# Kernel optimization log

Hardware: AMD Instinct MI355X
Metric: run time of the kernel (lower is better)

Reference implementation:

```python
import jax, jax.numpy as jnp
import numpy as np

D = 1024        # hidden_dim
E = 8           # num_experts
K = 2           # activated_experts
H = 4 * D       # ffn hidden


def setup_inputs() -> dict:
    key = jax.random.key(0)
    ks = jax.random.split(key, 12)
    s = 1.0 / np.sqrt(D)
    sh = 1.0 / np.sqrt(H)
    return {
        "x": jax.random.normal(ks[0], (2, 2048, D), dtype=jnp.float32),
        "gate_w": jax.random.uniform(ks[1], (D, E), minval=-s, maxval=s, dtype=jnp.float32),
        "gate_b": jax.random.uniform(ks[2], (E,), minval=-s, maxval=s, dtype=jnp.float32),
        "route_bias": jnp.zeros((E,), dtype=jnp.float32),
        "shared_w1": jax.random.uniform(ks[3], (D, H), minval=-s, maxval=s, dtype=jnp.float32),
        "shared_b1": jax.random.uniform(ks[4], (H,), minval=-s, maxval=s, dtype=jnp.float32),
        "shared_w2": jax.random.uniform(ks[5], (H, D), minval=-sh, maxval=sh, dtype=jnp.float32),
        "shared_b2": jax.random.uniform(ks[6], (D,), minval=-sh, maxval=sh, dtype=jnp.float32),
        "exp_w1": jax.random.uniform(ks[7], (E, D, H), minval=-s, maxval=s, dtype=jnp.float32),
        "exp_b1": jax.random.uniform(ks[8], (E, H), minval=-s, maxval=s, dtype=jnp.float32),
        "exp_w2": jax.random.uniform(ks[9], (E, H, D), minval=-sh, maxval=sh, dtype=jnp.float32),
        "exp_b2": jax.random.uniform(ks[10], (E, D), minval=-sh, maxval=sh, dtype=jnp.float32),
    }


def reference(x, gate_w, gate_b, route_bias, shared_w1, shared_b1, shared_w2,
              shared_b2, exp_w1, exp_b1, exp_w2, exp_b2):
    B, S, _ = x.shape
    xf = x.reshape(-1, D)                                  # [T, D]
    T = xf.shape[0]

    # Routing: gate logits + learned load-balancing bias -> softmax -> top-k
    gate_logits = xf @ gate_w + gate_b + route_bias        # [T, E]
    gate_probs = jax.nn.softmax(gate_logits, axis=-1)
    topk_p, topk_i = jax.lax.top_k(gate_probs, K)          # [T, K]
    topk_p = topk_p / jnp.sum(topk_p, axis=-1, keepdims=True)

    # Per-token combine weights over experts (zero for unselected experts)
    w = jnp.zeros((T, E), dtype=xf.dtype)
    w = w.at[jnp.arange(T)[:, None], topk_i].add(topk_p)   # [T, E]

    # Dense per-expert FFN (grouped GEMM form), weighted combine
    h = jax.nn.gelu(jnp.einsum('td,edh->eth', xf, exp_w1) + exp_b1[:, None, :],
                    approximate=False)                     # [E, T, H]
    y = jnp.einsum('eth,ehd->etd', h, exp_w2) + exp_b2[:, None, :]  # [E, T, D]
    combined = jnp.einsum('etd,te->td', y, w)              # [T, D]

    # Shared expert
    sh = jax.nn.gelu(xf @ shared_w1 + shared_b1, approximate=False)
    shared_out = sh @ shared_w2 + shared_b2                # [T, D]

    return (shared_out + combined).reshape(B, S, D)
```

## Files before the change

kernel.cpp:

```cpp
#include <hip/hip_runtime.h>
#include <math.h>

#define TT 4096
#define DD 1024
#define EE 8
#define HH 4096
#define NEXP 9

typedef __bf16 bf16;
typedef __bf16 bf16x4 __attribute__((ext_vector_type(4)));
typedef __bf16 bf16x8 __attribute__((ext_vector_type(8)));
typedef float  f32x4  __attribute__((ext_vector_type(4)));

#define GLOAD_LDS16(gptr, lptr)                                                   \
  __builtin_amdgcn_global_load_lds(                                               \
      (const __attribute__((address_space(1))) void*)(gptr),                      \
      (__attribute__((address_space(3))) void*)(lptr), 16, 0, 0)

__global__ void k_init(const float* __restrict__ x, bf16* __restrict__ xb,
                       float* __restrict__ out, int* __restrict__ counts,
                       int* __restrict__ cursors) {
  int i = blockIdx.x * blockDim.x + threadIdx.x;
  if (i < TT * DD) { xb[i] = (bf16)x[i]; out[i] = 0.0f; }
  if (i < EE) { counts[i] = 0; cursors[i] = 0; }
}

__global__ void k_route(const float* __restrict__ x, const float* __restrict__ gw,
                        const float* __restrict__ gb, const float* __restrict__ rb,
                        int* __restrict__ counts, int* __restrict__ tke,
                        float* __restrict__ tkp) {
  int gid = blockIdx.x * blockDim.x + threadIdx.x;
  int t = gid >> 6;
  int lane = gid & 63;
  if (t >= TT) return;
  const float* xt = x + (size_t)t * DD;
  float acc[EE];
#pragma unroll
  for (int e = 0; e < EE; e++) acc[e] = 0.f;
  for (int d = lane; d < DD; d += 64) {
    float xv = xt[d];
    const float* g = gw + (size_t)d * EE;
#pragma unroll
    for (int e = 0; e < EE; e++) acc[e] += xv * g[e];
  }
#pragma unroll
  for (int off = 32; off > 0; off >>= 1) {
#pragma unroll
    for (int e = 0; e < EE; e++) acc[e] += __shfl_down(acc[e], off);
  }
  if (lane == 0) {
    float l[EE];
#pragma unroll
    for (int e = 0; e < EE; e++) l[e] = acc[e] + gb[e] + rb[e];
    int i1 = 0;
#pragma unroll
    for (int e = 1; e < EE; e++) if (l[e] > l[i1]) i1 = e;
    int i2 = (i1 == 0) ? 1 : 0;
#pragma unroll
    for (int e = 0; e < EE; e++) if (e != i1 && l[e] > l[i2]) i2 = e;
    float e2 = expf(l[i2] - l[i1]);
    float s = 1.f + e2;
    tke[t * 2 + 0] = i1; tkp[t * 2 + 0] = 1.f / s;
    tke[t * 2 + 1] = i2; tkp[t * 2 + 1] = e2 / s;
    atomicAdd(&counts[i1], 1);
    atomicAdd(&counts[i2], 1);
  }
}

__global__ void k_prefix(const int* __restrict__ counts, int* __restrict__ expBase,
                         int* __restrict__ expCnt) {
  if (blockIdx.x == 0 && threadIdx.x == 0) {
    int off = TT;
    for (int e = 0; e < EE; e++) { expBase[e] = off; expCnt[e] = counts[e]; off += counts[e]; }
    expBase[8] = 0; expCnt[8] = TT;
  }
}

__global__ void k_scatter(const int* __restrict__ tke, const float* __restrict__ tkp,
                          const int* __restrict__ expBase, int* __restrict__ cursors,
                          int* __restrict__ rowTok, float* __restrict__ rowW) {
  int t = blockIdx.x * blockDim.x + threadIdx.x;
  if (t >= TT) return;
  rowTok[t] = t; rowW[t] = 1.f;
#pragma unroll
  for (int k = 0; k < 2; k++) {
    int e = tke[t * 2 + k];
    float p = tkp[t * 2 + k];
    int slot = atomicAdd(&cursors[e], 1);
    int r = expBase[e] + slot;
    rowTok[r] = t; rowW[r] = p;
  }
}

__global__ void k_wt(const float* __restrict__ expW, const float* __restrict__ shW,
                     bf16* __restrict__ outT, int K, int N) {
  __shared__ float t[64][65];
  int z = blockIdx.z;
  const float* W = (z == 8) ? shW : expW + (size_t)z * K * N;
  bf16* O = outT + (size_t)z * K * N;
  int n0 = blockIdx.x * 64, k0 = blockIdx.y * 64;
  int tid = threadIdx.x;
  int rr = tid >> 4;
  int cc = (tid & 15) * 4;
#pragma unroll
  for (int p = 0; p < 4; p++) {
    int k = p * 16 + rr;
    f32x4 v = *(const f32x4*)&W[(size_t)(k0 + k) * N + n0 + cc];
    t[k][cc + 0] = v[0]; t[k][cc + 1] = v[1]; t[k][cc + 2] = v[2]; t[k][cc + 3] = v[3];
  }
  __syncthreads();
#pragma unroll
  for (int p = 0; p < 4; p++) {
    int n = p * 16 + rr;
    bf16x4 o;
#pragma unroll
    for (int i = 0; i < 4; i++) o[i] = (bf16)t[cc + i][n];
    *(bf16x4*)&O[(size_t)(n0 + n) * K + k0 + cc] = o;
  }
}

__global__ __launch_bounds__(256, 2) void k_gemm1(
    const bf16* __restrict__ xb, const bf16* __restrict__ wt1,
    const float* __restrict__ sb1, const float* __restrict__ eb1,
    const int* __restrict__ rowTok, const int* __restrict__ expBase,
    const int* __restrict__ expCnt, bf16* __restrict__ hbuf) {
  int ex = blockIdx.z;
  int base = expBase[ex];
  int cnt  = expCnt[ex];
  int mt = blockIdx.y;
  if (mt * 128 >= cnt) return;
  int n0 = blockIdx.x * 128;
  const bf16* Bt = wt1 + (size_t)ex * HH * DD;
  const float* b1 = (ex == 8) ? sb1 : eb1 + (size_t)ex * HH;

  __shared__ bf16 As[128 * 32];
  __shared__ bf16 Bs[128 * 32];
  __shared__ int  toks[128];

  int tid = threadIdx.x;
  int lane = tid & 63;
  int wv = tid >> 6;
  int wm = (wv & 1) * 64;
  int wn = (wv >> 1) * 64;

  if (tid < 128) {
    int rr = min(mt * 128 + tid, cnt - 1);
    toks[tid] = rowTok[base + rr];
  }

  f32x4 acc[4][4];
#pragma unroll
  for (int a = 0; a < 4; a++)
#pragma unroll
    for (int b = 0; b < 4; b++) acc[a][b] = (f32x4){0.f, 0.f, 0.f, 0.f};

  __syncthreads();

  int r0 = wv * 32 + (lane >> 2);
  int c8 = (lane & 3) * 8;

  for (int k0 = 0; k0 < DD; k0 += 32) {
    GLOAD_LDS16(xb + (size_t)toks[r0] * DD + k0 + c8,      As + wv * 1024);
    GLOAD_LDS16(xb + (size_t)toks[r0 + 16] * DD + k0 + c8, As + wv * 1024 + 512);
    GLOAD_LDS16(Bt + (size_t)(n0 + r0) * DD + k0 + c8,      Bs + wv * 1024);
    GLOAD_LDS16(Bt + (size_t)(n0 + r0 + 16) * DD + k0 + c8, Bs + wv * 1024 + 512);
    __syncthreads();
    bf16x8 af[4], bfr[4];
#pragma unroll
    for (int mi = 0; mi < 4; mi++)
      af[mi] = *(const bf16x8*)&As[(wm + mi * 16 + (lane & 15)) * 32 + (lane >> 4) * 8];
#pragma unroll
    for (int ni = 0; ni < 4; ni++)
      bfr[ni] = *(const bf16x8*)&Bs[(wn + ni * 16 + (lane & 15)) * 32 + (lane >> 4) * 8];
#pragma unroll
    for (int mi = 0; mi < 4; mi++)
#pragma unroll
      for (int ni = 0; ni < 4; ni++)
        acc[mi][ni] = __builtin_amdgcn_mfma_f32_16x16x32_bf16(af[mi], bfr[ni], acc[mi][ni], 0, 0, 0);
    __syncthreads();
  }

  int rsub = (lane >> 4) * 4;
#pragma unroll
  for (int ni = 0; ni < 4; ni++) {
    int col = n0 + wn + ni * 16 + (lane & 15);
    float bias = b1[col];
#pragma unroll
    for (int mi = 0; mi < 4; mi++) {
#pragma unroll
      for (int r = 0; r < 4; r++) {
        int mrow = mt * 128 + wm + mi * 16 + rsub + r;
        if (mrow < cnt) {
          float v = acc[mi][ni][r] + bias;
          v = 0.5f * v * (1.f + erff(v * 0.70710678118654752f));
          hbuf[(size_t)(base + mrow) * HH + col] = (bf16)v;
        }
      }
    }
  }
}

__global__ __launch_bounds__(256, 2) void k_gemm2(
    const bf16* __restrict__ hbuf, const bf16* __restrict__ wt2,
    const float* __restrict__ sb2, const float* __restrict__ eb2,
    const int* __restrict__ rowTok, const float* __restrict__ rowW,
    const int* __restrict__ expBase, const int* __restrict__ expCnt,
    float* __restrict__ out) {
  int ex = blockIdx.z;
  int base = expBase[ex];
  int cnt  = expCnt[ex];
  int mt = blockIdx.y;
  if (mt * 128 >= cnt) return;
  int n0 = blockIdx.x * 128;
  const bf16* Bt = wt2 + (size_t)ex * DD * HH;
  const float* b2 = (ex == 8) ? sb2 : eb2 + (size_t)ex * DD;

  __shared__ bf16 As[128 * 32];
  __shared__ bf16 Bs[128 * 32];
  __shared__ int   toks[128];
  __shared__ float wrow[128];

  int tid = threadIdx.x;
  int lane = tid & 63;
  int wv = tid >> 6;
  int wm = (wv & 1) * 64;
  int wn = (wv >> 1) * 64;

  if (tid < 128) {
    int rr = min(mt * 128 + tid, cnt - 1);
    toks[tid] = rowTok[base + rr];
    wrow[tid] = rowW[base + rr];
  }

  f32x4 acc[4][4];
#pragma unroll
  for (int a = 0; a < 4; a++)
#pragma unroll
    for (int b = 0; b < 4; b++) acc[a][b] = (f32x4){0.f, 0.f, 0.f, 0.f};

  __syncthreads();

  int r0 = wv * 32 + (lane >> 2);
  int c8 = (lane & 3) * 8;
  int pr0 = base + min(mt * 128 + r0, cnt - 1);
  int pr1 = base + min(mt * 128 + r0 + 16, cnt - 1);
  const bf16* ga0 = hbuf + (size_t)pr0 * HH + c8;
  const bf16* ga1 = hbuf + (size_t)pr1 * HH + c8;

  for (int k0 = 0; k0 < HH; k0 += 32) {
    GLOAD_LDS16(ga0 + k0, As + wv * 1024);
    GLOAD_LDS16(ga1 + k0, As + wv * 1024 + 512);
    GLOAD_LDS16(Bt + (size_t)(n0 + r0) * HH + k0 + c8,      Bs + wv * 1024);
    GLOAD_LDS16(Bt + (size_t)(n0 + r0 + 16) * HH + k0 + c8, Bs + wv * 1024 + 512);
    __syncthreads();
    bf16x8 af[4], bfr[4];
#pragma unroll
    for (int mi = 0; mi < 4; mi++)
      af[mi] = *(const bf16x8*)&As[(wm + mi * 16 + (lane & 15)) * 32 + (lane >> 4) * 8];
#pragma unroll
    for (int ni = 0; ni < 4; ni++)
      bfr[ni] = *(const bf16x8*)&Bs[(wn + ni * 16 + (lane & 15)) * 32 + (lane >> 4) * 8];
#pragma unroll
    for (int mi = 0; mi < 4; mi++)
#pragma unroll
      for (int ni = 0; ni < 4; ni++)
        acc[mi][ni] = __builtin_amdgcn_mfma_f32_16x16x32_bf16(af[mi], bfr[ni], acc[mi][ni], 0, 0, 0);
    __syncthreads();
  }

  int rsub = (lane >> 4) * 4;
#pragma unroll
  for (int ni = 0; ni < 4; ni++) {
    int col = n0 + wn + ni * 16 + (lane & 15);
    float bias = b2[col];
#pragma unroll
    for (int mi = 0; mi < 4; mi++) {
#pragma unroll
      for (int r = 0; r < 4; r++) {
        int local = wm + mi * 16 + rsub + r;
        int mrow = mt * 128 + local;
        if (mrow < cnt) {
          float v = acc[mi][ni][r] + bias;
          atomicAdd(&out[(size_t)toks[local] * DD + col], wrow[local] * v);
        }
      }
    }
  }
}

extern "C" void kernel_launch(void* const* d_in, const int* in_sizes, int n_in,
                              void* d_out, int out_size, void* d_ws, size_t ws_size,
                              hipStream_t stream) {
  const float* x   = (const float*)d_in[0];
  const float* gw  = (const float*)d_in[1];
  const float* gb  = (const float*)d_in[2];
  const float* rb  = (const float*)d_in[3];
  const float* sw1 = (const float*)d_in[4];
  const float* sb1 = (const float*)d_in[5];
  const float* sw2 = (const float*)d_in[6];
  const float* sb2 = (const float*)d_in[7];
  const float* ew1 = (const float*)d_in[8];
  const float* eb1 = (const float*)d_in[9];
  const float* ew2 = (const float*)d_in[10];
  const float* eb2 = (const float*)d_in[11];
  float* out = (float*)d_out;

  char* p = (char*)d_ws;
  bf16* xb    = (bf16*)p;  p += (size_t)TT * DD * sizeof(bf16);
  bf16* hbuf  = (bf16*)p;  p += (size_t)(3 * TT) * HH * sizeof(bf16);
  bf16* wtb   = (bf16*)p;  p += (size_t)NEXP * DD * HH * sizeof(bf16);
  int* rowTok = (int*)p;   p += (size_t)(3 * TT) * sizeof(int);
  float* rowW = (float*)p; p += (size_t)(3 * TT) * sizeof(float);
  int* tke    = (int*)p;   p += (size_t)TT * 2 * sizeof(int);
  float* tkp  = (float*)p; p += (size_t)TT * 2 * sizeof(float);
  int* counts = (int*)p;   p += EE * sizeof(int);
  int* cursors= (int*)p;   p += EE * sizeof(int);
  int* expBase= (int*)p;   p += NEXP * sizeof(int);
  int* expCnt = (int*)p;   p += NEXP * sizeof(int);

  k_init<<<(TT * DD + 255) / 256, 256, 0, stream>>>(x, xb, out, counts, cursors);
  k_route<<<TT / 4, 256, 0, stream>>>(x, gw, gb, rb, counts, tke, tkp);
  k_prefix<<<1, 64, 0, stream>>>(counts, expBase, expCnt);
  k_scatter<<<TT / 256, 256, 0, stream>>>(tke, tkp, expBase, cursors, rowTok, rowW);

  dim3 gt1(HH / 64, DD / 64, NEXP);
  k_wt<<<gt1, 256, 0, stream>>>(ew1, sw1, wtb, DD, HH);
  dim3 g1(HH / 128, 32, NEXP);
  k_gemm1<<<g1, 256, 0, stream>>>(xb, wtb, sb1, eb1, rowTok, expBase, expCnt, hbuf);

  dim3 gt2(DD / 64, HH / 64, NEXP);
  k_wt<<<gt2, 256, 0, stream>>>(ew2, sw2, wtb, HH, DD);
  dim3 g2(DD / 128, 32, NEXP);
  k_gemm2<<<g2, 256, 0, stream>>>(hbuf, wtb, sb2, eb2, rowTok, rowW, expBase, expCnt, out);
}
```

Baseline: 906.1 us.

## Split-K the second expert GEMM and widen transpose kernel stores

The down-projection GEMM is split into two K halves, which doubles the number of blocks. Both halves accumulate into the output through the existing atomics, and only the first half adds the bias. The goal is to raise occupancy across the GPU, since the GEMM2 grid (8 N-tiles × up to ~16 M-tiles per expert) is small. Separately, the weight transpose/convert kernel now has each thread write 16 contiguous bf16 values as two 16-byte stores instead of 4-element stores, for better store coalescing. The cost is twice the atomic traffic on the output and a larger LDS bank-conflict pattern in the transpose read.

```diff
diff --git a/kernel.cpp b/kernel.cpp
--- a/kernel.cpp
+++ b/kernel.cpp
@@ -8,7 +8,6 @@
 #define NEXP 9
 
 typedef __bf16 bf16;
-typedef __bf16 bf16x4 __attribute__((ext_vector_type(4)));
 typedef __bf16 bf16x8 __attribute__((ext_vector_type(8)));
 typedef float  f32x4  __attribute__((ext_vector_type(4)));
 
@@ -92,31 +91,36 @@
   }
 }
 
-__global__ void k_wt(const float* __restrict__ expW, const float* __restrict__ shW,
-                     bf16* __restrict__ outT, int K, int N) {
+__global__ __launch_bounds__(256) void k_wt(const float* __restrict__ expW,
+                                            const float* __restrict__ shW,
+                                            bf16* __restrict__ outT, int K, int N) {
   __shared__ float t[64][65];
   int z = blockIdx.z;
   const float* W = (z == 8) ? shW : expW + (size_t)z * K * N;
   bf16* O = outT + (size_t)z * K * N;
   int n0 = blockIdx.x * 64, k0 = blockIdx.y * 64;
   int tid = threadIdx.x;
-  int rr = tid >> 4;
-  int cc = (tid & 15) * 4;
-#pragma unroll
-  for (int p = 0; p < 4; p++) {
-    int k = p * 16 + rr;
-    f32x4 v = *(const f32x4*)&W[(size_t)(k0 + k) * N + n0 + cc];
-    t[k][cc + 0] = v[0]; t[k][cc + 1] = v[1]; t[k][cc + 2] = v[2]; t[k][cc + 3] = v[3];
+  int kr = tid >> 2;
+  int cf = (tid & 3) * 16;
+#pragma unroll
+  for (int i = 0; i < 4; i++) {
+    f32x4 v = *(const f32x4*)&W[(size_t)(k0 + kr) * N + n0 + cf + i * 4];
+    t[kr][cf + i * 4 + 0] = v[0];
+    t[kr][cf + i * 4 + 1] = v[1];
+    t[kr][cf + i * 4 + 2] = v[2];
+    t[kr][cf + i * 4 + 3] = v[3];
   }
   __syncthreads();
-#pragma unroll
-  for (int p = 0; p < 4; p++) {
-    int n = p * 16 + rr;
-    bf16x4 o;
-#pragma unroll
-    for (int i = 0; i < 4; i++) o[i] = (bf16)t[cc + i][n];
-    *(bf16x4*)&O[(size_t)(n0 + n) * K + k0 + cc] = o;
-  }
+  int nr = tid >> 2;
+  int kf = (tid & 3) * 16;
+  bf16x8 o0, o1;
+#pragma unroll
+  for (int j = 0; j < 8; j++) o0[j] = (bf16)t[kf + j][nr];
+#pragma unroll
+  for (int j = 0; j < 8; j++) o1[j] = (bf16)t[kf + 8 + j][nr];
+  bf16* dst = O + (size_t)(n0 + nr) * K + k0 + kf;
+  *(bf16x8*)dst = o0;
+  *(bf16x8*)(dst + 8) = o1;
 }
 
 __global__ __launch_bounds__(256, 2) void k_gemm1(
@@ -209,7 +213,8 @@
   int ex = blockIdx.z;
   int base = expBase[ex];
   int cnt  = expCnt[ex];
-  int mt = blockIdx.y;
+  int ks = blockIdx.y & 1;
+  int mt = blockIdx.y >> 1;
   if (mt * 128 >= cnt) return;
   int n0 = blockIdx.x * 128;
   const bf16* Bt = wt2 + (size_t)ex * DD * HH;
@@ -247,7 +252,8 @@
   const bf16* ga0 = hbuf + (size_t)pr0 * HH + c8;
   const bf16* ga1 = hbuf + (size_t)pr1 * HH + c8;
 
-  for (int k0 = 0; k0 < HH; k0 += 32) {
+  int kbeg = ks * (HH / 2), kend = kbeg + (HH / 2);
+  for (int k0 = kbeg; k0 < kend; k0 += 32) {
     GLOAD_LDS16(ga0 + k0, As + wv * 1024);
     GLOAD_LDS16(ga1 + k0, As + wv * 1024 + 512);
     GLOAD_LDS16(Bt + (size_t)(n0 + r0) * HH + k0 + c8,      Bs + wv * 1024);
@@ -272,7 +278,7 @@
 #pragma unroll
   for (int ni = 0; ni < 4; ni++) {
     int col = n0 + wn + ni * 16 + (lane & 15);
-    float bias = b2[col];
+    float bias = (ks == 0) ? b2[col] : 0.f;
 #pragma unroll
     for (int mi = 0; mi < 4; mi++) {
 #pragma unroll
@@ -330,6 +336,6 @@
 
   dim3 gt2(DD / 64, HH / 64, NEXP);
   k_wt<<<gt2, 256, 0, stream>>>(ew2, sw2, wtb, HH, DD);
-  dim3 g2(DD / 128, 32, NEXP);
+  dim3 g2(DD / 128, 64, NEXP);
   k_gemm2<<<g2, 256, 0, stream>>>(hbuf, wtb, sb2, eb2, rowTok, rowW, expBase, expCnt, out);
 }
```

New measurement: 919.9 us. About the same (+1.5%).
